# Kernel optimization log

Measured on AMD Instinct MI355X. Metric: run time of the kernel, lower is better.

Reference implementation:

```python
import jax, jax.numpy as jnp
import numpy as np

K = 32          # kernel_size == per-unit image side
GRID = 128      # SOM grid side (units)
H = K * GRID    # full SOM canvas side = 4096
EPS = 1e-8      # variance-weighting stabilizer


def setup_inputs() -> dict:
    key = jax.random.key(0)
    k1, k2, k3 = jax.random.split(key, 3)
    input_image = jax.random.uniform(k1, (K, K), dtype=jnp.float32)
    som_matrix = jax.random.uniform(k2, (H, H), dtype=jnp.float32)
    # variances kept strictly positive
    som_running_variances = jax.random.uniform(k3, (H, H), dtype=jnp.float32) + 0.1
    return {
        "input_image": input_image,
        "som_matrix": som_matrix,
        "som_running_variances": som_running_variances,
    }


def _box_sum(x, k):
    """k x k stride-1 VALID box-sum via integral image (avoids O(N*k^2) patches)."""
    s = jnp.cumsum(jnp.cumsum(x, axis=0), axis=1)
    s = jnp.pad(s, ((1, 0), (1, 0)))  # [H+1, H+1]
    return s[k:, k:] - s[:-k, k:] - s[k:, :-k] + s[:-k, :-k]  # [H-k+1, H-k+1]


def reference(input_image, som_matrix, som_running_variances):
    # build(): kernel = tile(input_image, som_grid)
    kernel = jnp.tile(input_image, (H // K, H // K))  # [H, H]
    # util.global_variance_distance: variance-weighted squared distance per pixel
    dist = (kernel - som_matrix) ** 2 / (som_running_variances + EPS)  # [H, H]
    # stride-1 k x k patch extraction + per-patch sum == box filter
    return _box_sum(dist, K)  # [H-K+1, H-K+1]
```

## Files before the change

kernel.cpp:

```cpp
#include <hip/hip_runtime.h>
#include <hip/hip_bf16.h>

#define HH 4096
#define KK 32
#define OH 4065
#define NB 225
#define BC 256
#define RCHUNK 64
#define GR 8
#define NSUB (RCHUNK / GR)

__device__ __forceinline__ void barrier_lds_only() {
    asm volatile("" ::: "memory");
    __builtin_amdgcn_s_waitcnt(0xC07F);
    __builtin_amdgcn_s_barrier();
    asm volatile("" ::: "memory");
}

__global__ __launch_bounds__(BC, 4) void som_fused(
    const float* __restrict__ img,
    const float* __restrict__ som,
    const float* __restrict__ var,
    float* __restrict__ out)
{
    __shared__ float simg[KK * KK];
    __shared__ float ldsv[2][GR][BC];

    const int tid  = threadIdx.x;
    const int lane = tid & 63;
    const int wv   = tid >> 6;

    for (int i = tid; i < KK * KK; i += BC) simg[i] = img[i];
    __syncthreads();

    const int c0   = blockIdx.x * NB;
    const int col  = c0 + tid;
    const int colc = col < HH ? col : HH - 1;
    const int jc   = col & (KK - 1);
    const int r0   = blockIdx.y * RCHUNK;
    const int maxoff = HH - 1 - r0;

    const float* sp = som + (size_t)r0 * HH + colc;
    const float* vp = var + (size_t)r0 * HH + colc;

    float ring[KK];
    float sum = 0.f;
#pragma unroll
    for (int t = 0; t < KK; ++t) {
        const float s  = sp[t * HH];
        const float v  = vp[t * HH];
        const float im = simg[(t << 5) | jc];
        const float e  = im - s;
        const float d  = e * e * __builtin_amdgcn_rcpf(v + 1e-8f);
        ring[t] = d;
        sum += d;
    }

    float pf_s[2][GR], pf_v[2][GR];
#pragma unroll
    for (int k = 0; k < GR; ++k) {
        const int off = KK + k;
        pf_s[0][k] = sp[off * HH];
        pf_v[0][k] = vp[off * HH];
    }

#pragma unroll
    for (int sub = 0; sub < NSUB; ++sub) {
        const int buf = sub & 1;

#pragma unroll
        for (int k = 0; k < GR; ++k) {
            int off = KK + (sub + 1) * GR + k;
            off = off <= maxoff ? off : maxoff;
            pf_s[buf ^ 1][k] = sp[off * HH];
            pf_v[buf ^ 1][k] = vp[off * HH];
        }

#pragma unroll
        for (int k = 0; k < GR; ++k) {
            ldsv[buf][k][tid] = sum;
            const float s  = pf_s[buf][k];
            const float v  = pf_v[buf][k];
            const float im = simg[(((sub * GR + k) & (KK - 1)) << 5) | jc];
            const float e  = im - s;
            const float d  = e * e * __builtin_amdgcn_rcpf(v + 1e-8f);
            const int ri   = (sub * GR + k) & (KK - 1);
            sum += d - ring[ri];
            ring[ri] = d;
        }
        barrier_lds_only();

#pragma unroll
        for (int rr = 0; rr < 2; ++rr) {
            const int k = 2 * wv + rr;
            float4 x = *(const float4*)&ldsv[buf][k][lane * 4];
            const float p0 = x.x;
            const float p1 = p0 + x.y;
            const float p2 = p1 + x.z;
            const float p3 = p2 + x.w;
            float sc = p3;
#pragma unroll
            for (int off = 1; off < 64; off <<= 1) {
                const float t = __shfl_up(sc, off, 64);
                sc += (lane >= off) ? t : 0.f;
            }
            const float excl = sc - p3;
            float4 o;
            o.x = p0 + excl; o.y = p1 + excl; o.z = p2 + excl; o.w = p3 + excl;
            *(float4*)&ldsv[buf][k][lane * 4] = o;
        }
        barrier_lds_only();

        if (tid < NB && col < OH) {
#pragma unroll
            for (int k = 0; k < GR; ++k) {
                const int rout = r0 + sub * GR + k;
                if (rout < OH) {
                    const float hi = ldsv[buf][k][tid + KK - 1];
                    const float lo = (tid > 0) ? ldsv[buf][k][tid - 1] : 0.f;
                    out[(size_t)rout * OH + col] = hi - lo;
                }
            }
        }
    }
}

extern "C" void kernel_launch(void* const* d_in, const int* in_sizes, int n_in,
                              void* d_out, int out_size, void* d_ws, size_t ws_size,
                              hipStream_t stream) {
    (void)in_sizes; (void)n_in; (void)out_size; (void)d_ws; (void)ws_size;
    const float* img = (const float*)d_in[0];
    const float* som = (const float*)d_in[1];
    const float* var = (const float*)d_in[2];
    float* out = (float*)d_out;

    dim3 blk(BC);
    dim3 grd((OH + NB - 1) / NB,
             (OH + RCHUNK - 1) / RCHUNK);
    hipLaunchKernelGGL(som_fused, grd, blk, 0, stream, img, som, var, out);
}
```

Measured before the change: 200.2 us.

## Halve row chunk, compute box differences with shuffles, single LDS buffer

Row chunk shrinks from 64 to 32 and the launch bounds ask for 8 blocks per CU. Because a chunk is now exactly one ring period, the ring indexing simplifies and the last prefetch is skipped. The output stage no longer re-reads the scanned row from LDS: each lane builds the 32-wide window differences from cross-lane shuffles on its four prefix values, writes them straight to global, and the double-buffered LDS becomes a single buffer. The cost is that the 32-row ring warm-up is now paid for every 32 output rows instead of every 64, so loads of som and var roughly increase by half. Writes also become strided per lane, 4 floats each, which may coalesce worse.

```diff
diff --git a/kernel.cpp b/kernel.cpp
--- a/kernel.cpp
+++ b/kernel.cpp
@@ -6,7 +6,7 @@
 #define OH 4065
 #define NB 225
 #define BC 256
-#define RCHUNK 64
+#define RCHUNK 32
 #define GR 8
 #define NSUB (RCHUNK / GR)
 
@@ -17,14 +17,14 @@
     asm volatile("" ::: "memory");
 }
 
-__global__ __launch_bounds__(BC, 4) void som_fused(
+__global__ __launch_bounds__(BC, 8) void som_fused(
     const float* __restrict__ img,
     const float* __restrict__ som,
     const float* __restrict__ var,
     float* __restrict__ out)
 {
     __shared__ float simg[KK * KK];
-    __shared__ float ldsv[2][GR][BC];
+    __shared__ float ldsv[GR][BC];
 
     const int tid  = threadIdx.x;
     const int lane = tid & 63;
@@ -39,6 +39,7 @@
     const int jc   = col & (KK - 1);
     const int r0   = blockIdx.y * RCHUNK;
     const int maxoff = HH - 1 - r0;
+    const int cnt  = min(NB, OH - c0);
 
     const float* sp = som + (size_t)r0 * HH + colc;
     const float* vp = var + (size_t)r0 * HH + colc;
@@ -59,7 +60,8 @@
     float pf_s[2][GR], pf_v[2][GR];
 #pragma unroll
     for (int k = 0; k < GR; ++k) {
-        const int off = KK + k;
+        int off = KK + k;
+        off = off <= maxoff ? off : maxoff;
         pf_s[0][k] = sp[off * HH];
         pf_v[0][k] = vp[off * HH];
     }
@@ -68,32 +70,32 @@
     for (int sub = 0; sub < NSUB; ++sub) {
         const int buf = sub & 1;
 
+        if (sub + 1 < NSUB) {
 #pragma unroll
-        for (int k = 0; k < GR; ++k) {
-            int off = KK + (sub + 1) * GR + k;
-            off = off <= maxoff ? off : maxoff;
-            pf_s[buf ^ 1][k] = sp[off * HH];
-            pf_v[buf ^ 1][k] = vp[off * HH];
+            for (int k = 0; k < GR; ++k) {
+                int off = KK + (sub + 1) * GR + k;
+                off = off <= maxoff ? off : maxoff;
+                pf_s[buf ^ 1][k] = sp[off * HH];
+                pf_v[buf ^ 1][k] = vp[off * HH];
+            }
         }
 
 #pragma unroll
         for (int k = 0; k < GR; ++k) {
-            ldsv[buf][k][tid] = sum;
+            ldsv[k][tid] = sum;
             const float s  = pf_s[buf][k];
             const float v  = pf_v[buf][k];
-            const float im = simg[(((sub * GR + k) & (KK - 1)) << 5) | jc];
+            const float im = simg[((sub * GR + k) << 5) | jc];
             const float e  = im - s;
             const float d  = e * e * __builtin_amdgcn_rcpf(v + 1e-8f);
-            const int ri   = (sub * GR + k) & (KK - 1);
-            sum += d - ring[ri];
-            ring[ri] = d;
+            sum += d - ring[sub * GR + k];
         }
         barrier_lds_only();
 
 #pragma unroll
         for (int rr = 0; rr < 2; ++rr) {
             const int k = 2 * wv + rr;
-            float4 x = *(const float4*)&ldsv[buf][k][lane * 4];
+            float4 x = *(const float4*)&ldsv[k][lane * 4];
             const float p0 = x.x;
             const float p1 = p0 + x.y;
             const float p2 = p1 + x.z;
@@ -105,23 +107,27 @@
                 sc += (lane >= off) ? t : 0.f;
             }
             const float excl = sc - p3;
-            float4 o;
-            o.x = p0 + excl; o.y = p1 + excl; o.z = p2 + excl; o.w = p3 + excl;
-            *(float4*)&ldsv[buf][k][lane * 4] = o;
+            const float P0 = p0 + excl, P1 = p1 + excl;
+            const float P2 = p2 + excl, P3 = p3 + excl;
+
+            const float A  = __shfl_down(P3, 7, 64);
+            const float B0 = __shfl_down(P0, 8, 64);
+            const float B1 = __shfl_down(P1, 8, 64);
+            const float B2 = __shfl_down(P2, 8, 64);
+            float L = __shfl_up(P3, 1, 64);
+            L = (lane == 0) ? 0.f : L;
+
+            const int rout = r0 + sub * GR + k;
+            if (rout < OH) {
+                const int cb = lane * 4;
+                float* op = out + (size_t)rout * OH + c0 + cb;
+                if (cb + 0 < cnt) op[0] = A  - L;
+                if (cb + 1 < cnt) op[1] = B0 - P0;
+                if (cb + 2 < cnt) op[2] = B1 - P1;
+                if (cb + 3 < cnt) op[3] = B2 - P2;
+            }
         }
         barrier_lds_only();
-
-        if (tid < NB && col < OH) {
-#pragma unroll
-            for (int k = 0; k < GR; ++k) {
-                const int rout = r0 + sub * GR + k;
-                if (rout < OH) {
-                    const float hi = ldsv[buf][k][tid + KK - 1];
-                    const float lo = (tid > 0) ? ldsv[buf][k][tid - 1] : 0.f;
-                    out[(size_t)rout * OH + col] = hi - lo;
-                }
-            }
-        }
     }
 }
 
```

After: 296.7 us. 1.48x slower.
